# Kernel optimization log

Measured on AMD Instinct MI355X. Metric: run time of the kernel, lower is better.

Reference implementation:

```python
import jax, jax.numpy as jnp
import numpy as np

B, S, E, H, V, C = 64, 512, 256, 128, 50000, 2


def setup_inputs() -> dict:
    key = jax.random.key(0)
    ks = jax.random.split(key, 12)
    sentences = jax.random.randint(ks[0], (B, S), 0, V, dtype=jnp.int32)
    # sparse binary adjacency (dependency-tree-like), float for bmm
    adj = (jax.random.uniform(ks[1], (B, S, S)) < 0.05).astype(jnp.float32)
    emb_table = jax.random.normal(ks[2], (V, E), dtype=jnp.float32) * 0.02
    W1 = jax.random.normal(ks[3], (H, E), dtype=jnp.float32) * 0.05
    b1 = jnp.zeros((H,), jnp.float32)
    W2 = jax.random.normal(ks[4], (H, H), dtype=jnp.float32) * 0.05
    b2 = jnp.zeros((H,), jnp.float32)
    W3 = jax.random.normal(ks[5], (H, H), dtype=jnp.float32) * 0.05
    b3 = jnp.zeros((H,), jnp.float32)
    Wp = jax.random.normal(ks[6], (C, H), dtype=jnp.float32) * 0.05
    bp = jnp.zeros((C,), jnp.float32)
    return {"sentences": sentences, "adj": adj, "emb_table": emb_table,
            "W1": W1, "b1": b1, "W2": W2, "b2": b2, "W3": W3, "b3": b3,
            "Wp": Wp, "bp": bp}


def reference(sentences, adj, emb_table, W1, b1, W2, b2, W3, b3, Wp, bp):
    # embedding lookup (dropout is eval-mode identity)
    h = emb_table[sentences]  # [B, S, E]
    # degree normalization term (self-loop adds +1)
    deg = jnp.sum(adj, axis=-1, keepdims=True) + 1.0  # [B, S, 1]
    for W, b in ((W1, b1), (W2, b2), (W3, b3)):
        agg = jnp.einsum('bst,btd->bsd', adj, h)  # bmm(adj, h)
        # layer(agg) + layer(h) == (agg + h) @ W^T + 2b  (shared weights)
        h = ((agg + h) @ W.T + 2.0 * b) / deg
        h = jax.nn.relu(h)
    # AdaptiveMaxPool1d(1) over sequence dim
    pooled = jnp.max(h, axis=1)  # [B, H]
    logits = pooled @ Wp.T + bp  # [B, C]
    return logits
```

## Files before the change

### kernel.cpp

```cpp
#include <hip/hip_runtime.h>
#include <hip/hip_bf16.h>

typedef unsigned short ushort_t;

#define B_ 64
#define S_ 512
#define E_ 256
#define H_ 128
#define M_ (B_ * S_)
#define CAP_ 128


__global__ void k_adjidx(const float* __restrict__ adj,
                         ushort_t* __restrict__ idxl,
                         int* __restrict__ nnz,
                         float* __restrict__ invdeg) {
    int row  = blockIdx.x * 4 + (threadIdx.x >> 6);
    int lane = threadIdx.x & 63;
    const float4* arow = (const float4*)(adj + (size_t)row * S_);
    ushort_t* dst = idxl + (size_t)row * CAP_;
    int total = 0;
    #pragma unroll
    for (int c = 0; c < 2; ++c) {
        float4 v = arow[c * 64 + lane];
        float f[4] = {v.x, v.y, v.z, v.w};
        #pragma unroll
        for (int j = 0; j < 4; ++j) {
            unsigned long long m = __ballot(f[j] != 0.0f);
            if (f[j] != 0.0f) {
                int pos = total + __popcll(m & ((1ull << lane) - 1ull));
                if (pos < CAP_) dst[pos] = (ushort_t)(c * 256 + lane * 4 + j);
            }
            total += __popcll(m);
        }
    }
    if (lane == 0) {
        nnz[row] = total < CAP_ ? total : CAP_;
        invdeg[row] = 1.0f / (float)(total + 1);
    }
}

template <int K, bool GATHER>
__global__ __launch_bounds__(256, 2) void k_gemm(const float* __restrict__ X,
                                                 const int* __restrict__ sent,
                                                 const float* __restrict__ emb,
                                                 const float* __restrict__ W,
                                                 float* __restrict__ out) {
    __shared__ float Ws[128 * 68];
    __shared__ float Xs[4][16 * 36];
    int tid  = threadIdx.x;
    int wave = tid >> 6, lane = tid & 63;
    int rb      = blockIdx.x >> 1;
    int colBase = (blockIdx.x & 1) * 64;
    int rowBase = rb * 128 + wave * 32;

    int cc = lane & 15, rr = lane >> 4;
    int kg = lane & 3,  rowi = lane >> 2;

    const float* xs0;
    const float* xs1;
    if (GATHER) {
        xs0 = emb + (size_t)sent[rowBase + rowi]      * K + kg * 4;
        xs1 = emb + (size_t)sent[rowBase + rowi + 16] * K + kg * 4;
    } else {
        xs0 = X + (size_t)(rowBase + rowi)      * K + kg * 4;
        xs1 = X + (size_t)(rowBase + rowi + 16) * K + kg * 4;
    }

    float acc[8][4] = {};
    float* xsw = Xs[wave];

    for (int kh = 0; kh < K; kh += 128) {
        if (kh) __syncthreads();
        {
            int j  = tid & 63;
            int kq = tid >> 6;
            const float* wp = W + (size_t)(colBase + j) * K + kh + kq * 32;
            #pragma unroll
            for (int i = 0; i < 8; ++i) {
                float4 v = *(const float4*)(wp + i * 4);
                int k = kq * 32 + i * 4;
                Ws[(k + 0) * 68 + j] = v.x; Ws[(k + 1) * 68 + j] = v.y;
                Ws[(k + 2) * 68 + j] = v.z; Ws[(k + 3) * 68 + j] = v.w;
            }
        }
        float4 f0 = *(const float4*)(xs0 + kh);
        float4 f1 = *(const float4*)(xs1 + kh);
        __syncthreads();

        #pragma unroll 1
        for (int kk = 0; kk < 128; kk += 16) {
            xsw[(kg * 4 + 0) * 36 + rowi] = f0.x;
            xsw[(kg * 4 + 1) * 36 + rowi] = f0.y;
            xsw[(kg * 4 + 2) * 36 + rowi] = f0.z;
            xsw[(kg * 4 + 3) * 36 + rowi] = f0.w;
            xsw[(kg * 4 + 0) * 36 + rowi + 16] = f1.x;
            xsw[(kg * 4 + 1) * 36 + rowi + 16] = f1.y;
            xsw[(kg * 4 + 2) * 36 + rowi + 16] = f1.z;
            xsw[(kg * 4 + 3) * 36 + rowi + 16] = f1.w;
            if (kk + 16 < 128) {
                f0 = *(const float4*)(xs0 + kh + kk + 16);
                f1 = *(const float4*)(xs1 + kh + kk + 16);
            }
            #pragma unroll
            for (int k = 0; k < 16; ++k) {
                float4 a0 = *(const float4*)&xsw[k * 36 + rr * 8];
                float4 a1 = *(const float4*)&xsw[k * 36 + rr * 8 + 4];
                float4 wv = *(const float4*)&Ws[(kk + k) * 68 + cc * 4];
                float xv[8] = {a0.x, a0.y, a0.z, a0.w, a1.x, a1.y, a1.z, a1.w};
                #pragma unroll
                for (int i = 0; i < 8; ++i) {
                    acc[i][0] += xv[i] * wv.x;
                    acc[i][1] += xv[i] * wv.y;
                    acc[i][2] += xv[i] * wv.z;
                    acc[i][3] += xv[i] * wv.w;
                }
            }
        }
    }

    #pragma unroll
    for (int i = 0; i < 8; ++i) {
        int row = rowBase + rr * 8 + i;
        float4 o = {acc[i][0], acc[i][1], acc[i][2], acc[i][3]};
        *(float4*)(out + (size_t)row * H_ + colBase + cc * 4) = o;
    }
}

template <bool POOL>
__global__ __launch_bounds__(256) void k_aggf(const float* __restrict__ Y,
                                              const ushort_t* __restrict__ idxl,
                                              const int* __restrict__ nnz,
                                              const float* __restrict__ invdeg,
                                              const float* __restrict__ bias,
                                              float* __restrict__ out) {
    int x    = blockIdx.x;
    int xcd  = x & 7;
    int slot = x >> 3;
    int b    = xcd + 8 * (slot >> 6);
    int g    = slot & 63;
    int r    = threadIdx.x >> 5;
    int row  = b * S_ + g * 8 + r;
    int c    = threadIdx.x & 31;

    const float4* Y4 = (const float4*)Y;
    int n = nnz[row];
    const ushort_t* il = idxl + (size_t)row * CAP_;
    float4 acc = Y4[(size_t)row * 32 + c];
    float4 acc2 = {0.f, 0.f, 0.f, 0.f};
    size_t base = (size_t)b * S_ * 32;

    int i = 0;
    for (; i + 4 <= n; i += 4) {
        int t0 = il[i], t1 = il[i + 1], t2 = il[i + 2], t3 = il[i + 3];
        float4 v0 = Y4[base + (size_t)t0 * 32 + c];
        float4 v1 = Y4[base + (size_t)t1 * 32 + c];
        float4 v2 = Y4[base + (size_t)t2 * 32 + c];
        float4 v3 = Y4[base + (size_t)t3 * 32 + c];
        acc.x += v0.x + v1.x; acc.y += v0.y + v1.y;
        acc.z += v0.z + v1.z; acc.w += v0.w + v1.w;
        acc2.x += v2.x + v3.x; acc2.y += v2.y + v3.y;
        acc2.z += v2.z + v3.z; acc2.w += v2.w + v3.w;
    }
    for (; i < n; ++i) {
        int t = il[i];
        float4 v = Y4[base + (size_t)t * 32 + c];
        acc.x += v.x; acc.y += v.y; acc.z += v.z; acc.w += v.w;
    }
    acc.x += acc2.x; acc.y += acc2.y; acc.z += acc2.z; acc.w += acc2.w;

    float inv = invdeg[row];
    float4 bv = ((const float4*)bias)[c];
    float4 o;
    o.x = fmaxf((acc.x + 2.0f * bv.x) * inv, 0.0f);
    o.y = fmaxf((acc.y + 2.0f * bv.y) * inv, 0.0f);
    o.z = fmaxf((acc.z + 2.0f * bv.z) * inv, 0.0f);
    o.w = fmaxf((acc.w + 2.0f * bv.w) * inv, 0.0f);

    if (!POOL) {
        ((float4*)out)[(size_t)row * 32 + c] = o;
    } else {
        __shared__ float4 sm[8][33];
        sm[r][c] = o;
        __syncthreads();
        if (r == 0) {
            float4 m = sm[0][c];
            #pragma unroll
            for (int q = 1; q < 8; ++q) {
                float4 v = sm[q][c];
                m.x = fmaxf(m.x, v.x); m.y = fmaxf(m.y, v.y);
                m.z = fmaxf(m.z, v.z); m.w = fmaxf(m.w, v.w);
            }
            ((float4*)out)[((size_t)b * 64 + g) * 32 + c] = m;
        }
    }
}

__global__ void k_final(const float* __restrict__ pp,
                        const float* __restrict__ Wp,
                        const float* __restrict__ bp,
                        float* __restrict__ out) {
    int b = blockIdx.x, j = threadIdx.x;
    const float* p = pp + (size_t)b * 64 * H_ + j;
    float m = -1e30f;
    #pragma unroll 8
    for (int i = 0; i < 64; ++i) m = fmaxf(m, p[(size_t)i * H_]);
    float t0 = m * Wp[j];
    float t1 = m * Wp[H_ + j];
    #pragma unroll
    for (int off = 32; off > 0; off >>= 1) {
        t0 += __shfl_down(t0, off);
        t1 += __shfl_down(t1, off);
    }
    __shared__ float red[2][2];
    int wave = j >> 6, lane = j & 63;
    if (lane == 0) { red[0][wave] = t0; red[1][wave] = t1; }
    __syncthreads();
    if (j == 0) out[b * 2 + 0] = red[0][0] + red[0][1] + bp[0];
    if (j == 1) out[b * 2 + 1] = red[1][0] + red[1][1] + bp[1];
}

extern "C" void kernel_launch(void* const* d_in, const int* in_sizes, int n_in,
                              void* d_out, int out_size, void* d_ws, size_t ws_size,
                              hipStream_t stream) {
    const int*   sent = (const int*)d_in[0];
    const float* adj  = (const float*)d_in[1];
    const float* emb  = (const float*)d_in[2];
    const float* W1   = (const float*)d_in[3];
    const float* b1   = (const float*)d_in[4];
    const float* W2   = (const float*)d_in[5];
    const float* b2   = (const float*)d_in[6];
    const float* W3   = (const float*)d_in[7];
    const float* b3   = (const float*)d_in[8];
    const float* Wp   = (const float*)d_in[9];
    const float* bp   = (const float*)d_in[10];
    float* out = (float*)d_out;

    char* ws = (char*)d_ws;
    float*    Ybuf   = (float*)ws;
    float*    h1     = (float*)(ws + ((size_t)16 << 20));
    float*    h2     = (float*)(ws + ((size_t)32 << 20));
    char*     base   = ws + ((size_t)48 << 20);
    float*    invdeg = (float*)base;
    int*      nnz    = (int*)(base + (size_t)M_ * 4);
    ushort_t* idxl   = (ushort_t*)(base + (size_t)M_ * 8);
    float*    pp     = (float*)(base + (size_t)M_ * 8 + (size_t)M_ * CAP_ * 2);

    k_adjidx<<<M_ / 4, 256, 0, stream>>>(adj, idxl, nnz, invdeg);

    k_gemm<E_, true ><<<512, 256, 0, stream>>>(nullptr, sent, emb, W1, Ybuf);
    k_aggf<false><<<M_ / 8, 256, 0, stream>>>(Ybuf, idxl, nnz, invdeg, b1, h1);

    k_gemm<H_, false><<<512, 256, 0, stream>>>(h1, nullptr, nullptr, W2, Ybuf);
    k_aggf<false><<<M_ / 8, 256, 0, stream>>>(Ybuf, idxl, nnz, invdeg, b2, h2);

    k_gemm<H_, false><<<512, 256, 0, stream>>>(h2, nullptr, nullptr, W3, Ybuf);
    k_aggf<true ><<<M_ / 8, 256, 0, stream>>>(Ybuf, idxl, nnz, invdeg, b3, pp);

    k_final<<<B_, H_, 0, stream>>>(pp, Wp, bp, out);
}
```

Baseline: 296.7 us.

## Fuse per-layer GEMM and neighbor aggregation into one LDS-resident kernel

Replaces the separate GEMM and gather-aggregation kernels with one kernel per layer. Each block computes a 512-row x 32-column slice of X·W^T for one batch into shared memory, then aggregates neighbors from LDS. Pooling is folded into the last layer. This removes the global round-trip of the intermediate Y and the global gathers. In exchange it uses about 107KB of LDS per block, allowing one block per CU with 256 blocks total, and re-reads input rows once per column group.

```diff
diff --git a/kernel.cpp b/kernel.cpp
--- a/kernel.cpp
+++ b/kernel.cpp
@@ -1,5 +1,4 @@
 #include <hip/hip_runtime.h>
-#include <hip/hip_bf16.h>
 
 typedef unsigned short ushort_t;
 
@@ -9,7 +8,6 @@
 #define H_ 128
 #define M_ (B_ * S_)
 #define CAP_ 128
-
 
 __global__ void k_adjidx(const float* __restrict__ adj,
                          ushort_t* __restrict__ idxl,
@@ -40,171 +38,190 @@
     }
 }
 
-template <int K, bool GATHER>
-__global__ __launch_bounds__(256, 2) void k_gemm(const float* __restrict__ X,
-                                                 const int* __restrict__ sent,
-                                                 const float* __restrict__ emb,
-                                                 const float* __restrict__ W,
-                                                 float* __restrict__ out) {
-    __shared__ float Ws[128 * 68];
-    __shared__ float Xs[4][16 * 36];
-    int tid  = threadIdx.x;
-    int wave = tid >> 6, lane = tid & 63;
-    int rb      = blockIdx.x >> 1;
-    int colBase = (blockIdx.x & 1) * 64;
-    int rowBase = rb * 128 + wave * 32;
-
-    int cc = lane & 15, rr = lane >> 4;
-    int kg = lane & 3,  rowi = lane >> 2;
-
-    const float* xs0;
-    const float* xs1;
-    if (GATHER) {
-        xs0 = emb + (size_t)sent[rowBase + rowi]      * K + kg * 4;
-        xs1 = emb + (size_t)sent[rowBase + rowi + 16] * K + kg * 4;
-    } else {
-        xs0 = X + (size_t)(rowBase + rowi)      * K + kg * 4;
-        xs1 = X + (size_t)(rowBase + rowi + 16) * K + kg * 4;
-    }
-
-    float acc[8][4] = {};
-    float* xsw = Xs[wave];
-
-    for (int kh = 0; kh < K; kh += 128) {
-        if (kh) __syncthreads();
-        {
-            int j  = tid & 63;
-            int kq = tid >> 6;
-            const float* wp = W + (size_t)(colBase + j) * K + kh + kq * 32;
+template <int K, bool GATHER, bool POOL>
+__global__ __launch_bounds__(256, 1)
+void k_layer(const float* __restrict__ X, const int* __restrict__ sent,
+             const float* __restrict__ emb, const float* __restrict__ W,
+             const ushort_t* __restrict__ idxl, const int* __restrict__ nnz,
+             const float* __restrict__ invdeg, const float* __restrict__ bias,
+             float* __restrict__ out) {
+    __shared__ __align__(16) float Ys[S_ * 36];
+    __shared__ __align__(16) float Xs[2][8 * S_];
+    __shared__ __align__(16) float Wsh[2][8 * 32];
+
+    const int tid = threadIdx.x;
+    const int bid = blockIdx.x;
+    const int xcd = bid & 7, slot = bid >> 3;
+    const int b = xcd + 8 * (slot >> 2);
+    const int cg = slot & 3;
+    const int colBase = cg * 32;
+    const int rowBase = b * S_;
+
+    const int row0 = tid >> 1;
+    const int kq   = (tid & 1) * 4;
+    const float* xp[4];
+    #pragma unroll
+    for (int q = 0; q < 4; ++q) {
+        const int r = row0 + 128 * q;
+        const float* src;
+        if (GATHER) src = emb + (size_t)sent[rowBase + r] * K;
+        else        src = X + (size_t)(rowBase + r) * K;
+        xp[q] = src + kq;
+    }
+    const int wcol = (tid >> 1) & 31;
+    const float* wp = W + (size_t)(colBase + wcol) * K + kq;
+
+    const int rg4 = tid & ~3;
+    const int c0  = (tid & 3) * 8;
+
+    float acc[8][8] = {};
+    float4 g[4];
+    float4 wv = {0.f, 0.f, 0.f, 0.f};
+
+    constexpr int NC = K / 8;
+
+    #pragma unroll
+    for (int q = 0; q < 4; ++q) g[q] = *(const float4*)(xp[q]);
+    if (tid < 64) wv = *(const float4*)(wp);
+    #pragma unroll
+    for (int q = 0; q < 4; ++q) {
+        const int pr = row0 + 128 * q;
+        Xs[0][(kq + 0) * 512 + pr] = g[q].x;
+        Xs[0][(kq + 1) * 512 + pr] = g[q].y;
+        Xs[0][(kq + 2) * 512 + pr] = g[q].z;
+        Xs[0][(kq + 3) * 512 + pr] = g[q].w;
+    }
+    if (tid < 64) {
+        Wsh[0][(kq + 0) * 32 + wcol] = wv.x;
+        Wsh[0][(kq + 1) * 32 + wcol] = wv.y;
+        Wsh[0][(kq + 2) * 32 + wcol] = wv.z;
+        Wsh[0][(kq + 3) * 32 + wcol] = wv.w;
+    }
+    __syncthreads();
+
+    #pragma unroll 1
+    for (int c = 0; c < NC; ++c) {
+        const int cur = c & 1;
+        if (c + 1 < NC) {
             #pragma unroll
-            for (int i = 0; i < 8; ++i) {
-                float4 v = *(const float4*)(wp + i * 4);
-                int k = kq * 32 + i * 4;
-                Ws[(k + 0) * 68 + j] = v.x; Ws[(k + 1) * 68 + j] = v.y;
-                Ws[(k + 2) * 68 + j] = v.z; Ws[(k + 3) * 68 + j] = v.w;
-            }
-        }
-        float4 f0 = *(const float4*)(xs0 + kh);
-        float4 f1 = *(const float4*)(xs1 + kh);
+            for (int q = 0; q < 4; ++q) g[q] = *(const float4*)(xp[q] + (c + 1) * 8);
+            if (tid < 64) wv = *(const float4*)(wp + (c + 1) * 8);
+        }
+        #pragma unroll
+        for (int k = 0; k < 8; ++k) {
+            const float4 xa = *(const float4*)&Xs[cur][k * 512 + rg4];
+            const float4 xb = *(const float4*)&Xs[cur][k * 512 + 256 + rg4];
+            const float4 wa = *(const float4*)&Wsh[cur][k * 32 + c0];
+            const float4 wb = *(const float4*)&Wsh[cur][k * 32 + c0 + 4];
+            const float xv[8]  = {xa.x, xa.y, xa.z, xa.w, xb.x, xb.y, xb.z, xb.w};
+            const float wv8[8] = {wa.x, wa.y, wa.z, wa.w, wb.x, wb.y, wb.z, wb.w};
+            #pragma unroll
+            for (int i = 0; i < 8; ++i)
+                #pragma unroll
+                for (int j = 0; j < 8; ++j)
+                    acc[i][j] += xv[i] * wv8[j];
+        }
+        if (c + 1 < NC) {
+            const int nb = cur ^ 1;
+            #pragma unroll
+            for (int q = 0; q < 4; ++q) {
+                const int pr = row0 + 128 * q;
+                Xs[nb][(kq + 0) * 512 + pr] = g[q].x;
+                Xs[nb][(kq + 1) * 512 + pr] = g[q].y;
+                Xs[nb][(kq + 2) * 512 + pr] = g[q].z;
+                Xs[nb][(kq + 3) * 512 + pr] = g[q].w;
+            }
+            if (tid < 64) {
+                Wsh[nb][(kq + 0) * 32 + wcol] = wv.x;
+                Wsh[nb][(kq + 1) * 32 + wcol] = wv.y;
+                Wsh[nb][(kq + 2) * 32 + wcol] = wv.z;
+                Wsh[nb][(kq + 3) * 32 + wcol] = wv.w;
+            }
+        }
         __syncthreads();
-
-        #pragma unroll 1
-        for (int kk = 0; kk < 128; kk += 16) {
-            xsw[(kg * 4 + 0) * 36 + rowi] = f0.x;
-            xsw[(kg * 4 + 1) * 36 + rowi] = f0.y;
-            xsw[(kg * 4 + 2) * 36 + rowi] = f0.z;
-            xsw[(kg * 4 + 3) * 36 + rowi] = f0.w;
-            xsw[(kg * 4 + 0) * 36 + rowi + 16] = f1.x;
-            xsw[(kg * 4 + 1) * 36 + rowi + 16] = f1.y;
-            xsw[(kg * 4 + 2) * 36 + rowi + 16] = f1.z;
-            xsw[(kg * 4 + 3) * 36 + rowi + 16] = f1.w;
-            if (kk + 16 < 128) {
-                f0 = *(const float4*)(xs0 + kh + kk + 16);
-                f1 = *(const float4*)(xs1 + kh + kk + 16);
-            }
-            #pragma unroll
-            for (int k = 0; k < 16; ++k) {
-                float4 a0 = *(const float4*)&xsw[k * 36 + rr * 8];
-                float4 a1 = *(const float4*)&xsw[k * 36 + rr * 8 + 4];
-                float4 wv = *(const float4*)&Ws[(kk + k) * 68 + cc * 4];
-                float xv[8] = {a0.x, a0.y, a0.z, a0.w, a1.x, a1.y, a1.z, a1.w};
-                #pragma unroll
-                for (int i = 0; i < 8; ++i) {
-                    acc[i][0] += xv[i] * wv.x;
-                    acc[i][1] += xv[i] * wv.y;
-                    acc[i][2] += xv[i] * wv.z;
-                    acc[i][3] += xv[i] * wv.w;
-                }
-            }
-        }
     }
 
     #pragma unroll
     for (int i = 0; i < 8; ++i) {
-        int row = rowBase + rr * 8 + i;
-        float4 o = {acc[i][0], acc[i][1], acc[i][2], acc[i][3]};
-        *(float4*)(out + (size_t)row * H_ + colBase + cc * 4) = o;
-    }
-}
-
-template <bool POOL>
-__global__ __launch_bounds__(256) void k_aggf(const float* __restrict__ Y,
-                                              const ushort_t* __restrict__ idxl,
-                                              const int* __restrict__ nnz,
-                                              const float* __restrict__ invdeg,
-                                              const float* __restrict__ bias,
-                                              float* __restrict__ out) {
-    int x    = blockIdx.x;
-    int xcd  = x & 7;
-    int slot = x >> 3;
-    int b    = xcd + 8 * (slot >> 6);
-    int g    = slot & 63;
-    int r    = threadIdx.x >> 5;
-    int row  = b * S_ + g * 8 + r;
-    int c    = threadIdx.x & 31;
-
-    const float4* Y4 = (const float4*)Y;
-    int n = nnz[row];
-    const ushort_t* il = idxl + (size_t)row * CAP_;
-    float4 acc = Y4[(size_t)row * 32 + c];
-    float4 acc2 = {0.f, 0.f, 0.f, 0.f};
-    size_t base = (size_t)b * S_ * 32;
-
-    int i = 0;
-    for (; i + 4 <= n; i += 4) {
-        int t0 = il[i], t1 = il[i + 1], t2 = il[i + 2], t3 = il[i + 3];
-        float4 v0 = Y4[base + (size_t)t0 * 32 + c];
-        float4 v1 = Y4[base + (size_t)t1 * 32 + c];
-        float4 v2 = Y4[base + (size_t)t2 * 32 + c];
-        float4 v3 = Y4[base + (size_t)t3 * 32 + c];
-        acc.x += v0.x + v1.x; acc.y += v0.y + v1.y;
-        acc.z += v0.z + v1.z; acc.w += v0.w + v1.w;
-        acc2.x += v2.x + v3.x; acc2.y += v2.y + v3.y;
-        acc2.z += v2.z + v3.z; acc2.w += v2.w + v3.w;
-    }
-    for (; i < n; ++i) {
-        int t = il[i];
-        float4 v = Y4[base + (size_t)t * 32 + c];
-        acc.x += v.x; acc.y += v.y; acc.z += v.z; acc.w += v.w;
-    }
-    acc.x += acc2.x; acc.y += acc2.y; acc.z += acc2.z; acc.w += acc2.w;
-
-    float inv = invdeg[row];
-    float4 bv = ((const float4*)bias)[c];
-    float4 o;
-    o.x = fmaxf((acc.x + 2.0f * bv.x) * inv, 0.0f);
-    o.y = fmaxf((acc.y + 2.0f * bv.y) * inv, 0.0f);
-    o.z = fmaxf((acc.z + 2.0f * bv.z) * inv, 0.0f);
-    o.w = fmaxf((acc.w + 2.0f * bv.w) * inv, 0.0f);
-
-    if (!POOL) {
-        ((float4*)out)[(size_t)row * 32 + c] = o;
-    } else {
-        __shared__ float4 sm[8][33];
-        sm[r][c] = o;
+        const int r = (i < 4) ? (rg4 + i) : (256 + rg4 + i - 4);
+        *(float4*)&Ys[r * 36 + c0]     = make_float4(acc[i][0], acc[i][1], acc[i][2], acc[i][3]);
+        *(float4*)&Ys[r * 36 + c0 + 4] = make_float4(acc[i][4], acc[i][5], acc[i][6], acc[i][7]);
+    }
+    __syncthreads();
+
+    const int rsub = tid >> 3;
+    const int cc   = tid & 7;
+    const float4* Ys4 = (const float4*)Ys;
+    const float4 bv = *(const float4*)(bias + colBase + cc * 4);
+    float4 pmax = {0.f, 0.f, 0.f, 0.f};
+
+    #pragma unroll 1
+    for (int p = 0; p < 16; ++p) {
+        const int r = p * 32 + rsub;
+        const int grow = rowBase + r;
+        const int n = nnz[grow];
+        const ushort_t* il = idxl + (size_t)grow * CAP_;
+        float4 a = Ys4[r * 9 + cc];
+        float4 a2 = {0.f, 0.f, 0.f, 0.f};
+        int i = 0;
+        for (; i + 4 <= n; i += 4) {
+            const unsigned long long pk = *(const unsigned long long*)(il + i);
+            const int t0 = (int)(pk & 0xffffu);
+            const int t1 = (int)((pk >> 16) & 0xffffu);
+            const int t2 = (int)((pk >> 32) & 0xffffu);
+            const int t3 = (int)((pk >> 48) & 0xffffu);
+            const float4 v0 = Ys4[t0 * 9 + cc];
+            const float4 v1 = Ys4[t1 * 9 + cc];
+            const float4 v2 = Ys4[t2 * 9 + cc];
+            const float4 v3 = Ys4[t3 * 9 + cc];
+            a.x += v0.x + v1.x;  a.y += v0.y + v1.y;
+            a.z += v0.z + v1.z;  a.w += v0.w + v1.w;
+            a2.x += v2.x + v3.x; a2.y += v2.y + v3.y;
+            a2.z += v2.z + v3.z; a2.w += v2.w + v3.w;
+        }
+        for (; i < n; ++i) {
+            const int t = il[i];
+            const float4 v = Ys4[t * 9 + cc];
+            a.x += v.x; a.y += v.y; a.z += v.z; a.w += v.w;
+        }
+        a.x += a2.x; a.y += a2.y; a.z += a2.z; a.w += a2.w;
+        const float inv = invdeg[grow];
+        float4 o;
+        o.x = fmaxf((a.x + 2.0f * bv.x) * inv, 0.0f);
+        o.y = fmaxf((a.y + 2.0f * bv.y) * inv, 0.0f);
+        o.z = fmaxf((a.z + 2.0f * bv.z) * inv, 0.0f);
+        o.w = fmaxf((a.w + 2.0f * bv.w) * inv, 0.0f);
+        if (!POOL) {
+            *(float4*)(out + (size_t)grow * H_ + colBase + cc * 4) = o;
+        } else {
+            pmax.x = fmaxf(pmax.x, o.x); pmax.y = fmaxf(pmax.y, o.y);
+            pmax.z = fmaxf(pmax.z, o.z); pmax.w = fmaxf(pmax.w, o.w);
+        }
+    }
+
+    if (POOL) {
+        float4* smax = (float4*)Xs;
+        smax[rsub * 8 + cc] = pmax;
         __syncthreads();
-        if (r == 0) {
-            float4 m = sm[0][c];
-            #pragma unroll
-            for (int q = 1; q < 8; ++q) {
-                float4 v = sm[q][c];
+        if (tid < 8) {
+            float4 m = smax[tid];
+            #pragma unroll 8
+            for (int q = 1; q < 32; ++q) {
+                const float4 v = smax[q * 8 + tid];
                 m.x = fmaxf(m.x, v.x); m.y = fmaxf(m.y, v.y);
                 m.z = fmaxf(m.z, v.z); m.w = fmaxf(m.w, v.w);
             }
-            ((float4*)out)[((size_t)b * 64 + g) * 32 + c] = m;
-        }
-    }
-}
-
-__global__ void k_final(const float* __restrict__ pp,
+            *(float4*)(out + (size_t)b * H_ + colBase + tid * 4) = m;
+        }
+    }
+}
+
+__global__ void k_final(const float* __restrict__ pooled,
                         const float* __restrict__ Wp,
                         const float* __restrict__ bp,
                         float* __restrict__ out) {
     int b = blockIdx.x, j = threadIdx.x;
-    const float* p = pp + (size_t)b * 64 * H_ + j;
-    float m = -1e30f;
-    #pragma unroll 8
-    for (int i = 0; i < 64; ++i) m = fmaxf(m, p[(size_t)i * H_]);
+    float m = pooled[(size_t)b * H_ + j];
     float t0 = m * Wp[j];
     float t1 = m * Wp[H_ + j];
     #pragma unroll
@@ -237,25 +254,19 @@
     float* out = (float*)d_out;
 
     char* ws = (char*)d_ws;
-    float*    Ybuf   = (float*)ws;
-    float*    h1     = (float*)(ws + ((size_t)16 << 20));
-    float*    h2     = (float*)(ws + ((size_t)32 << 20));
-    char*     base   = ws + ((size_t)48 << 20);
+    float*    h1     = (float*)ws;
+    float*    h2     = (float*)(ws + ((size_t)16 << 20));
+    char*     base   = ws + ((size_t)32 << 20);
     float*    invdeg = (float*)base;
     int*      nnz    = (int*)(base + (size_t)M_ * 4);
     ushort_t* idxl   = (ushort_t*)(base + (size_t)M_ * 8);
-    float*    pp     = (float*)(base + (size_t)M_ * 8 + (size_t)M_ * CAP_ * 2);
+    float*    pooled = (float*)(base + (size_t)M_ * 8 + (size_t)M_ * CAP_ * 2);
 
     k_adjidx<<<M_ / 4, 256, 0, stream>>>(adj, idxl, nnz, invdeg);
 
-    k_gemm<E_, true ><<<512, 256, 0, stream>>>(nullptr, sent, emb, W1, Ybuf);
-    k_aggf<false><<<M_ / 8, 256, 0, stream>>>(Ybuf, idxl, nnz, invdeg, b1, h1);
-
-    k_gemm<H_, false><<<512, 256, 0, stream>>>(h1, nullptr, nullptr, W2, Ybuf);
-    k_aggf<false><<<M_ / 8, 256, 0, stream>>>(Ybuf, idxl, nnz, invdeg, b2, h2);
-
-    k_gemm<H_, false><<<512, 256, 0, stream>>>(h2, nullptr, nullptr, W3, Ybuf);
-    k_aggf<true ><<<M_ / 8, 256, 0, stream>>>(Ybuf, idxl, nnz, invdeg, b3, pp);
-
-    k_final<<<B_, H_, 0, stream>>>(pp, Wp, bp, out);
-}
+    k_layer<E_, true,  false><<<256, 256, 0, stream>>>(nullptr, sent, emb, W1, idxl, nnz, invdeg, b1, h1);
+    k_layer<H_, false, false><<<256, 256, 0, stream>>>(h1, nullptr, nullptr, W2, idxl, nnz, invdeg, b2, h2);
+    k_layer<H_, false, true ><<<256, 256, 0, stream>>>(h2, nullptr, nullptr, W3, idxl, nnz, invdeg, b3, pooled);
+
+    k_final<<<B_, H_, 0, stream>>>(pooled, Wp, bp, out);
+}
```

Result: slower. 326.8 us (+10.2%).
